# Kernel optimization log

Hardware: AMD Instinct MI355X
Metric: run time of the kernel (lower is better)

Reference implementation:

```python
import jax, jax.numpy as jnp
import numpy as np

HID, FFN, E, K = 1024, 4096, 8, 2
CAP_FACTOR = 1.25


def setup_inputs() -> dict:
    key = jax.random.key(0)
    k1, k2, k3, k4 = jax.random.split(key, 4)
    B, T = 4, 2048
    x = jax.random.normal(k1, (B, T, HID), dtype=jnp.float32)
    router_w = jax.random.normal(k2, (E, HID), dtype=jnp.float32) * 0.02
    w1 = jax.random.normal(k3, (E, HID, FFN), dtype=jnp.float32) * 0.02
    w2 = jax.random.normal(k4, (E, FFN, HID), dtype=jnp.float32) * 0.02
    return {"x": x, "router_w": router_w, "w1": w1, "w2": w2}


def reference(x, router_w, w1, w2):
    B, T, H = x.shape
    N = B * T
    x_flat = x.reshape(N, H)
    # capacity per expert (static, shape-derived)
    C = max(1, int(CAP_FACTOR * N / E * K))

    # router (eval mode: no noise)
    logits = x_flat @ router_w.T                      # [N, E]
    probs = jax.nn.softmax(logits, axis=-1)
    top_v, top_i = jax.lax.top_k(probs, K)            # [N, K]
    top_v = top_v / jnp.sum(top_v, axis=-1, keepdims=True)

    out = jnp.zeros_like(x_flat)
    for k in range(K):
        eid = top_i[:, k]                             # [N] expert id per token
        gate = top_v[:, k]                            # [N]
        # position of each token within its expert, in token order
        onehot = jax.nn.one_hot(eid, E, dtype=jnp.int32)          # [N, E]
        pos = jnp.take_along_axis(jnp.cumsum(onehot, axis=0), eid[:, None], axis=1)[:, 0] - 1
        keep = pos < C                                # capacity drop (first C in token order)
        slot = jnp.where(keep, eid * C + pos, E * C)  # dropped tokens -> dump slot

        # dispatch: scatter kept tokens into per-expert capacity buffers
        buf = jnp.zeros((E * C + 1, H), dtype=x.dtype).at[slot].add(
            x_flat * keep[:, None].astype(x.dtype))
        expert_in = buf[: E * C].reshape(E, C, H)     # [E, C, H]

        # per-expert FFN (grouped GEMM -> GELU -> grouped GEMM)
        h = jax.nn.gelu(jnp.einsum('ech,ehf->ecf', expert_in, w1), approximate=False)
        y = jnp.einsum('ecf,efh->ech', h, w2)         # [E, C, H]

        # combine: gather back to token order, mask dropped, apply gate
        tok = y.reshape(E * C, H)[jnp.minimum(slot, E * C - 1)]
        out = out + tok * (gate * keep.astype(x.dtype))[:, None]

    return out.reshape(B, T, H)
```

## Files before the change

kernel.cpp:

```cpp
#include <hip/hip_runtime.h>
#include <hip/hip_bf16.h>
#include <math.h>

#define N_TOK 8192
#define HIDD  1024
#define FFND  4096
#define NE    8
#define CAP   2560
#define TMX   20
#define RMAX  16512
#define PBLK  128

typedef __attribute__((ext_vector_type(4))) float  f32x4;
typedef __attribute__((ext_vector_type(8))) __bf16 bf16x8;

__device__ __forceinline__ unsigned short f2bf(float f) {
    unsigned u = __float_as_uint(f);
    u = (u + 0x7fffu + ((u >> 16) & 1u)) >> 16;
    return (unsigned short)u;
}

__device__ __forceinline__ void gld_lds16(const void* g, void* l) {
    __builtin_amdgcn_global_load_lds(
        (const __attribute__((address_space(1))) unsigned int*)g,
        (__attribute__((address_space(3))) unsigned int*)l, 16, 0, 0);
}

template <int R, int C>
__global__ __launch_bounds__(256) void transpose_cvt(const float* __restrict__ W,
                                                     unsigned short* __restrict__ Wt) {
    __shared__ unsigned short st[64][72];
    int e  = blockIdx.z;
    int r0 = blockIdx.y * 64, c0 = blockIdx.x * 64;
    int tid = threadIdx.x;
    int rb = tid >> 4, cq = tid & 15;
    const float* src = W + ((size_t)e * R + r0) * C + c0;
#pragma unroll
    for (int i = 0; i < 4; i++) {
        int kr = i * 16 + rb;
        float4 v = *reinterpret_cast<const float4*>(src + (size_t)kr * C + cq * 4);
        st[cq * 4 + 0][kr] = f2bf(v.x);
        st[cq * 4 + 1][kr] = f2bf(v.y);
        st[cq * 4 + 2][kr] = f2bf(v.z);
        st[cq * 4 + 3][kr] = f2bf(v.w);
    }
    __syncthreads();
    unsigned short* dst = Wt + ((size_t)e * C + c0) * R + r0;
#pragma unroll
    for (int i = 0; i < 4; i++) {
        int cr = i * 16 + rb;
        uint2 v = *reinterpret_cast<const uint2*>(&st[cr][cq * 4]);
        *reinterpret_cast<uint2*>(dst + (size_t)cr * R + cq * 4) = v;
    }
}

__global__ __launch_bounds__(256) void router_kernel(const float* __restrict__ x,
                                                     const float* __restrict__ rw,
                                                     unsigned short* __restrict__ xbf,
                                                     int* __restrict__ cnt,
                                                     int* __restrict__ tok,
                                                     float* __restrict__ gate) {
    __shared__ float4 rwl[2048];
    __shared__ int   e0s[32], e1s[32];
    __shared__ float g0s[32], g1s[32];
    __shared__ int   baseS[16];

    int tid = threadIdx.x, lane = tid & 63, w = tid >> 6;
    for (int i = tid; i < 2048; i += 256) rwl[i] = reinterpret_cast<const float4*>(rw)[i];
    __syncthreads();

    int tbase = blockIdx.x * 32 + w * 8;
    for (int i = 0; i < 8; i++) {
        int t = tbase + i;
        const float4* xr = reinterpret_cast<const float4*>(x) + (size_t)t * 256;
        float4 xv[4];
#pragma unroll
        for (int c = 0; c < 4; c++) xv[c] = xr[c * 64 + lane];
        uint2* xb = reinterpret_cast<uint2*>(xbf) + (size_t)t * 256;
#pragma unroll
        for (int c = 0; c < 4; c++) {
            uint2 p;
            p.x = (unsigned)f2bf(xv[c].x) | ((unsigned)f2bf(xv[c].y) << 16);
            p.y = (unsigned)f2bf(xv[c].z) | ((unsigned)f2bf(xv[c].w) << 16);
            xb[c * 64 + lane] = p;
        }
        float dot[NE];
#pragma unroll
        for (int e = 0; e < NE; e++) {
            float s = 0.f;
#pragma unroll
            for (int c = 0; c < 4; c++) {
                float4 a = rwl[e * 256 + c * 64 + lane];
                s += xv[c].x * a.x + xv[c].y * a.y + xv[c].z * a.z + xv[c].w * a.w;
            }
            dot[e] = s;
        }
#pragma unroll
        for (int e = 0; e < NE; e++) {
            float v = dot[e];
#pragma unroll
            for (int o = 32; o > 0; o >>= 1) v += __shfl_xor(v, o, 64);
            dot[e] = v;
        }
        if (lane == 0) {
            int e0 = 0; float l0 = dot[0];
#pragma unroll
            for (int e = 1; e < NE; e++) if (dot[e] > l0) { l0 = dot[e]; e0 = e; }
            int e1 = -1; float l1 = -3.4e38f;
#pragma unroll
            for (int e = 0; e < NE; e++) if (e != e0 && dot[e] > l1) { l1 = dot[e]; e1 = e; }
            float g0 = 1.f / (1.f + expf(l1 - l0));
            int j = w * 8 + i;
            e0s[j] = e0; e1s[j] = e1; g0s[j] = g0; g1s[j] = 1.f - g0;
        }
    }
    __syncthreads();

    int e0 = 255, e1 = 255, rank0 = 0, rank1 = 0, slotcnt = 0;
    float g0 = 0.f, g1 = 0.f;
    if (w == 0) {
        if (lane < 32) { e0 = e0s[lane]; e1 = e1s[lane]; g0 = g0s[lane]; g1 = g1s[lane]; }
        unsigned long long lt = (1ull << lane) - 1ull;
#pragma unroll
        for (int ee = 0; ee < NE; ee++) {
            unsigned long long m0 = __ballot(e0 == ee);
            unsigned long long m1 = __ballot(e1 == ee);
            if (e0 == ee) rank0 = (int)__popcll(m0 & lt);
            if (e1 == ee) rank1 = (int)__popcll(m1 & lt);
            if (lane == ee)      slotcnt = (int)__popcll(m0);
            if (lane == NE + ee) slotcnt = (int)__popcll(m1);
        }
        if (lane < 16) baseS[lane] = atomicAdd(&cnt[lane * 16], slotcnt);
    }
    __syncthreads();
    if (w == 0 && lane < 32) {
        int t = blockIdx.x * 32 + lane;
        int p0 = baseS[e0] + rank0;
        if (p0 < CAP) { tok[e0 * CAP + p0] = t; gate[e0 * CAP + p0] = g0; }
        int p1 = baseS[NE + e1] + rank1;
        if (p1 < CAP) { tok[(NE + e1) * CAP + p1] = t; gate[(NE + e1) * CAP + p1] = g1; }
    }
}

template <int KD, int ND, int KS, int CH, bool G1>
__global__ __launch_bounds__(256, 4) void ffn_gemm_p(const unsigned short* __restrict__ A,
                                                     const unsigned short* __restrict__ Bw,
                                                     unsigned short* __restrict__ H,
                                                     float* __restrict__ O,
                                                     const int* __restrict__ cntAll,
                                                     const int* __restrict__ tokL,
                                                     const float* __restrict__ gateL) {
    constexpr int TN    = ND / 128;
    constexpr int UNITS = TN * KS;
    constexpr int KDS   = KD / KS;

    __shared__ __align__(16) unsigned short At[128 * 32];
    __shared__ __align__(16) unsigned short Bt[128 * 32];

    int e  = blockIdx.x & 7;
    int pb = blockIdx.x >> 3;

    int cnt0 = min(cntAll[e * 16], CAP);
    int cnt1 = min(cntAll[(e + 8) * 16], CAP);
    int tmx0 = (cnt0 + 127) >> 7, tmx1 = (cnt1 + 127) >> 7;
    int tmsum = tmx0 + tmx1;
    if (tmsum == 0) return;
    int per_chunk = tmsum * CH;
    int total = tmsum * UNITS;

    int offA = 0, offB = 0;
#pragma unroll
    for (int t = 0; t < 16; t++) {
        int cc = min(cntAll[t * 16], CAP);
        if (t < e)     offA += cc;
        if (t < e + 8) offB += cc;
    }

    int tid = threadIdx.x;
    int w = tid >> 6, l = tid & 63;
    int wr = w >> 1, wc = w & 1;

    int r1 = tid >> 2, q1 = tid & 3;
    int r2 = r1 + 64;
    int sw1 = ((q1 ^ ((r1 >> 1) & 3)) << 4);
    int sw2 = ((q1 ^ ((r2 >> 1) & 3)) << 4);
    char* aDst1 = (char*)At + w * 1024;
    char* aDst2 = aDst1 + 4096;
    char* bDst1 = (char*)Bt + w * 1024;
    char* bDst2 = bDst1 + 4096;

    int aro[4], bro[4];
#pragma unroll
    for (int m = 0; m < 4; m++) {
        int rr = wr * 64 + m * 16 + (l & 15);
        aro[m] = rr * 64 + (((l >> 4) ^ ((rr >> 1) & 3)) << 4);
        int cc = wc * 64 + m * 16 + (l & 15);
        bro[m] = cc * 64 + (((l >> 4) ^ ((cc >> 1) & 3)) << 4);
    }

    for (int u0 = pb; u0 < total; u0 += PBLK) {
        int c = u0 / per_chunk;
        int r = u0 - c * per_chunk;
        int s, tm, cnt_e, off_e;
        if (r < tmx0 * CH) { s = e;     tm = r / CH; r -= tm * CH; cnt_e = cnt0; off_e = offA; }
        else { r -= tmx0 * CH; s = e + 8; tm = r / CH; r -= tm * CH; cnt_e = cnt1; off_e = offB; }
        int u  = c * CH + r;
        int tn = (KS > 1) ? (u / KS) : u;
        int ks = (KS > 1) ? (u % KS) : 0;
        const int lbase = s * CAP;

        const char* aSrc1;
        const char* aSrc2;
        if (G1) {
            int p1 = tm * 128 + r1, p2 = tm * 128 + r2;
            int t1 = tokL[lbase + (p1 < cnt_e ? p1 : 0)];
            int t2 = tokL[lbase + (p2 < cnt_e ? p2 : 0)];
            aSrc1 = (const char*)(A + (size_t)t1 * KD + ks * KDS) + sw1;
            aSrc2 = (const char*)(A + (size_t)t2 * KD + ks * KDS) + sw2;
        } else {
            size_t row1 = (size_t)off_e + tm * 128 + r1;
            aSrc1 = (const char*)(A + row1 * KD + ks * KDS) + sw1;
            aSrc2 = (const char*)(A + (row1 + 64) * KD + ks * KDS) + sw2;
        }
        const char* bSrc1 = (const char*)(Bw + ((size_t)e * ND + tn * 128 + r1) * KD + ks * KDS) + sw1;
        const char* bSrc2 = (const char*)(Bw + ((size_t)e * ND + tn * 128 + r2) * KD + ks * KDS) + sw2;

        f32x4 acc[4][4];
#pragma unroll
        for (int m = 0; m < 4; m++)
#pragma unroll
            for (int n = 0; n < 4; n++) acc[m][n] = (f32x4){0.f, 0.f, 0.f, 0.f};

        for (int k0 = 0; k0 < KDS; k0 += 32) {
            size_t kb = (size_t)k0 * 2;
            gld_lds16(aSrc1 + kb, aDst1);
            gld_lds16(aSrc2 + kb, aDst2);
            gld_lds16(bSrc1 + kb, bDst1);
            gld_lds16(bSrc2 + kb, bDst2);
            __syncthreads();
            bf16x8 af[4], bf[4];
#pragma unroll
            for (int m = 0; m < 4; m++) af[m] = *reinterpret_cast<const bf16x8*>((const char*)At + aro[m]);
#pragma unroll
            for (int n = 0; n < 4; n++) bf[n] = *reinterpret_cast<const bf16x8*>((const char*)Bt + bro[n]);
#pragma unroll
            for (int m = 0; m < 4; m++)
#pragma unroll
                for (int n = 0; n < 4; n++)
                    acc[m][n] = __builtin_amdgcn_mfma_f32_16x16x32_bf16(af[m], bf[n], acc[m][n], 0, 0, 0);
            __syncthreads();
        }

        if (G1) {
#pragma unroll
            for (int m = 0; m < 4; m++) {
#pragma unroll
                for (int j = 0; j < 4; j++) {
                    int rr = wr * 64 + m * 16 + (l >> 4) * 4 + j;
                    int p = tm * 128 + rr;
                    if (p < cnt_e) {
                        unsigned short* hp = H + (size_t)(off_e + p) * ND + tn * 128 + wc * 64 + (l & 15);
#pragma unroll
                        for (int n = 0; n < 4; n++) {
                            float v = acc[m][n][j];
                            float g = 0.5f * v * (1.f + erff(v * 0.70710678118654752f));
                            hp[n * 16] = f2bf(g);
                        }
                    }
                }
            }
        } else {
#pragma unroll
            for (int m = 0; m < 4; m++) {
#pragma unroll
                for (int j = 0; j < 4; j++) {
                    int rr = wr * 64 + m * 16 + (l >> 4) * 4 + j;
                    int p = tm * 128 + rr;
                    if (p < cnt_e) {
                        int t = tokL[lbase + p];
                        float gv = gateL[lbase + p];
                        float* op = O + (size_t)t * ND + tn * 128 + wc * 64 + (l & 15);
#pragma unroll
                        for (int n = 0; n < 4; n++) atomicAdd(op + n * 16, gv * acc[m][n][j]);
                    }
                }
            }
        }
    }
}

template <int KD, int ND, bool G1>
__global__ __launch_bounds__(256) void ffn_gemm(const unsigned short* __restrict__ A,
                                                const float* __restrict__ W,
                                                unsigned short* __restrict__ H,
                                                float* __restrict__ O,
                                                const int* __restrict__ cntAll,
                                                const int* __restrict__ tokL,
                                                const float* __restrict__ gateL,
                                                int slot0, int pbase) {
    constexpr int TN = ND / 128;
    int bid = blockIdx.x;
    int tn  = bid % TN;
    int tme = bid / TN;
    int tm  = tme % TMX;
    int s   = slot0 + tme / TMX;
    int eW  = s & 7;
    int cnt_e = min(cntAll[s * 16], CAP);
    if (tm * 128 >= cnt_e) return;
    int off_e = 0;
#pragma unroll
    for (int i = 0; i < 16; i++) {
        int c = min(cntAll[i * 16], CAP);
        off_e += (i >= pbase && i < s) ? c : 0;
    }
    const int lbase = s * CAP;

    __shared__ __align__(16) unsigned short At[128 * 32];
    __shared__ __align__(16) unsigned short Bt[128 * 32];

    int tid = threadIdx.x;
    int w = tid >> 6, l = tid & 63;
    int wr = w >> 1, wc = w & 1;

    int r1 = tid >> 2, q1 = tid & 3;
    int r2 = r1 + 64;
    const char* aSrc1;
    const char* aSrc2;
    if (G1) {
        int p1 = tm * 128 + r1, p2 = tm * 128 + r2;
        int t1 = tokL[lbase + (p1 < cnt_e ? p1 : 0)];
        int t2 = tokL[lbase + (p2 < cnt_e ? p2 : 0)];
        aSrc1 = (const char*)(A + (size_t)t1 * KD) + ((q1 ^ ((r1 >> 1) & 3)) << 4);
        aSrc2 = (const char*)(A + (size_t)t2 * KD) + ((q1 ^ ((r2 >> 1) & 3)) << 4);
    } else {
        size_t row1 = (size_t)off_e + tm * 128 + r1;
        size_t row2 = row1 + 64;
        aSrc1 = (const char*)(A + row1 * KD) + ((q1 ^ ((r1 >> 1) & 3)) << 4);
        aSrc2 = (const char*)(A + row2 * KD) + ((q1 ^ ((r2 >> 1) & 3)) << 4);
    }
    char* aDst1 = (char*)At + w * 1024;
    char* aDst2 = aDst1 + 4096;

    const float* bSrc[4];
    int bOff[16];
#pragma unroll
    for (int j = 0; j < 4; j++) {
        int fidx = j * 1024 + tid * 4;
        int kk = fidx >> 7, n = fidx & 127;
        bSrc[j] = W + (size_t)eW * KD * ND + (size_t)kk * ND + tn * 128 + n;
#pragma unroll
        for (int i = 0; i < 4; i++) {
            int nn = n + i;
            bOff[j * 4 + i] = nn * 64 + ((((kk >> 3) ^ ((nn >> 1) & 3))) << 4) + ((kk & 7) << 1);
        }
    }

    int aro[4], bro[4];
#pragma unroll
    for (int m = 0; m < 4; m++) {
        int rr = wr * 64 + m * 16 + (l & 15);
        aro[m] = rr * 64 + (((l >> 4) ^ ((rr >> 1) & 3)) << 4);
        int cc = wc * 64 + m * 16 + (l & 15);
        bro[m] = cc * 64 + (((l >> 4) ^ ((cc >> 1) & 3)) << 4);
    }

    f32x4 zf = {0.f, 0.f, 0.f, 0.f};
    f32x4 acc[4][4];
#pragma unroll
    for (int m = 0; m < 4; m++)
#pragma unroll
        for (int n = 0; n < 4; n++) acc[m][n] = zf;

    for (int k0 = 0; k0 < KD; k0 += 32) {
        gld_lds16(aSrc1 + (size_t)k0 * 2, aDst1);
        gld_lds16(aSrc2 + (size_t)k0 * 2, aDst2);
        float4 bv[4];
#pragma unroll
        for (int j = 0; j < 4; j++) bv[j] = *reinterpret_cast<const float4*>(bSrc[j] + (size_t)k0 * ND);
        char* btc = (char*)Bt;
#pragma unroll
        for (int j = 0; j < 4; j++) {
            *(unsigned short*)(btc + bOff[j * 4 + 0]) = f2bf(bv[j].x);
            *(unsigned short*)(btc + bOff[j * 4 + 1]) = f2bf(bv[j].y);
            *(unsigned short*)(btc + bOff[j * 4 + 2]) = f2bf(bv[j].z);
            *(unsigned short*)(btc + bOff[j * 4 + 3]) = f2bf(bv[j].w);
        }
        __syncthreads();
        bf16x8 af[4], bf[4];
#pragma unroll
        for (int m = 0; m < 4; m++) af[m] = *reinterpret_cast<const bf16x8*>((const char*)At + aro[m]);
#pragma unroll
        for (int n = 0; n < 4; n++) bf[n] = *reinterpret_cast<const bf16x8*>((const char*)Bt + bro[n]);
#pragma unroll
        for (int m = 0; m < 4; m++)
#pragma unroll
            for (int n = 0; n < 4; n++)
                acc[m][n] = __builtin_amdgcn_mfma_f32_16x16x32_bf16(af[m], bf[n], acc[m][n], 0, 0, 0);
        __syncthreads();
    }

    if (G1) {
#pragma unroll
        for (int m = 0; m < 4; m++) {
#pragma unroll
            for (int j = 0; j < 4; j++) {
                int rr = wr * 64 + m * 16 + (l >> 4) * 4 + j;
                int p = tm * 128 + rr;
                if (p < cnt_e) {
                    size_t row = (size_t)(off_e + p);
                    unsigned short* hp = H + row * ND + tn * 128 + wc * 64 + (l & 15);
#pragma unroll
                    for (int n = 0; n < 4; n++) {
                        float v = acc[m][n][j];
                        float g = 0.5f * v * (1.f + erff(v * 0.70710678118654752f));
                        hp[n * 16] = f2bf(g);
                    }
                }
            }
        }
    } else {
#pragma unroll
        for (int m = 0; m < 4; m++) {
#pragma unroll
            for (int j = 0; j < 4; j++) {
                int rr = wr * 64 + m * 16 + (l >> 4) * 4 + j;
                int p = tm * 128 + rr;
                if (p < cnt_e) {
                    int t = tokL[lbase + p];
                    float gv = gateL[lbase + p];
                    float* op = O + (size_t)t * ND + tn * 128 + wc * 64 + (l & 15);
#pragma unroll
                    for (int n = 0; n < 4; n++) atomicAdd(op + n * 16, gv * acc[m][n][j]);
                }
            }
        }
    }
}

extern "C" void kernel_launch(void* const* d_in, const int* in_sizes, int n_in,
                              void* d_out, int out_size, void* d_ws, size_t ws_size,
                              hipStream_t stream) {
    const float* x  = (const float*)d_in[0];
    const float* rw = (const float*)d_in[1];
    const float* w1 = (const float*)d_in[2];
    const float* w2 = (const float*)d_in[3];
    float* out = (float*)d_out;
    char* ws = (char*)d_ws;

    int*   cnt  = (int*)ws;
    int*   tok  = (int*)(ws + 4096);
    float* gate = (float*)(ws + 4096 + 16 * CAP * 4);
    unsigned short* xbf = (unsigned short*)(ws + (1 << 20));
    size_t hOff = (1 << 20) + (size_t)N_TOK * HIDD * 2;
    unsigned short* h = (unsigned short*)(ws + hOff);

    size_t w1tSz = (size_t)NE * HIDD * FFND * 2;
    size_t hBig = (size_t)RMAX * FFND * 2;
    size_t needBig = hOff + hBig + 2 * w1tSz;

    hipMemsetAsync(cnt, 0, 1024, stream);
    hipMemsetAsync(d_out, 0, (size_t)N_TOK * HIDD * 4, stream);

    hipLaunchKernelGGL(router_kernel, dim3(N_TOK / 32), dim3(256), 0, stream,
                       x, rw, xbf, cnt, tok, gate);

    if (ws_size >= needBig) {
        unsigned short* w1t = (unsigned short*)(ws + hOff + hBig);
        unsigned short* w2t = (unsigned short*)(ws + hOff + hBig + w1tSz);
        hipLaunchKernelGGL((transpose_cvt<HIDD, FFND>), dim3(FFND / 64, HIDD / 64, NE), dim3(256), 0, stream, w1, w1t);
        hipLaunchKernelGGL((transpose_cvt<FFND, HIDD>), dim3(HIDD / 64, FFND / 64, NE), dim3(256), 0, stream, w2, w2t);
        hipLaunchKernelGGL((ffn_gemm_p<HIDD, FFND, 1, 8, true>), dim3(8 * PBLK), dim3(256), 0, stream,
                           xbf, w1t, h, (float*)nullptr, cnt, tok, gate);
        hipLaunchKernelGGL((ffn_gemm_p<FFND, HIDD, 2, 4, false>), dim3(8 * PBLK), dim3(256), 0, stream,
                           h, w2t, (unsigned short*)nullptr, out, cnt, tok, gate);
    } else {
        for (int k = 0; k < 2; k++) {
            hipLaunchKernelGGL((ffn_gemm<HIDD, FFND, true>), dim3(8 * TMX * (FFND / 128)), dim3(256), 0, stream,
                               xbf, w1, h, (float*)nullptr, cnt, tok, gate, 8 * k, 8 * k);
            hipLaunchKernelGGL((ffn_gemm<FFND, HIDD, false>), dim3(8 * TMX * (HIDD / 128)), dim3(256), 0, stream,
                               h, w2, (unsigned short*)nullptr, out, cnt, tok, gate, 8 * k, 8 * k);
        }
    }
}
```

Measured before the change: 542.1 us.

## Replace atomic down-proj combine with two ordered store/add passes and polynomial GELU

```diff
diff --git a/kernel.cpp b/kernel.cpp
--- a/kernel.cpp
+++ b/kernel.cpp
@@ -10,6 +10,7 @@
 #define TMX   20
 #define RMAX  16512
 #define PBLK  128
+#define PBLK2 64
 
 typedef __attribute__((ext_vector_type(4))) float  f32x4;
 typedef __attribute__((ext_vector_type(8))) __bf16 bf16x8;
@@ -18,6 +19,17 @@
     unsigned u = __float_as_uint(f);
     u = (u + 0x7fffu + ((u >> 16) & 1u)) >> 16;
     return (unsigned short)u;
+}
+
+__device__ __forceinline__ float gelu_f(float v) {
+    float x  = v * 0.70710678118654752f;
+    float ax = fabsf(x);
+    float t  = 1.0f / (1.0f + 0.3275911f * ax);
+    float poly = ((((1.061405429f * t - 1.453152027f) * t + 1.421413741f) * t
+                   - 0.284496736f) * t + 0.254829592f) * t;
+    float er = 1.0f - poly * __expf(-x * x);
+    er = copysignf(er, x);
+    return 0.5f * v * (1.0f + er);
 }
 
 __device__ __forceinline__ void gld_lds16(const void* g, void* l) {
@@ -142,14 +154,12 @@
     }
 }
 
-template <int KD, int ND, int KS, int CH, bool G1>
+template <int KD, int ND, int KS, int CH>
 __global__ __launch_bounds__(256, 4) void ffn_gemm_p(const unsigned short* __restrict__ A,
                                                      const unsigned short* __restrict__ Bw,
                                                      unsigned short* __restrict__ H,
-                                                     float* __restrict__ O,
                                                      const int* __restrict__ cntAll,
-                                                     const int* __restrict__ tokL,
-                                                     const float* __restrict__ gateL) {
+                                                     const int* __restrict__ tokL) {
     constexpr int TN    = ND / 128;
     constexpr int UNITS = TN * KS;
     constexpr int KDS   = KD / KS;
@@ -211,16 +221,12 @@
 
         const char* aSrc1;
         const char* aSrc2;
-        if (G1) {
+        {
             int p1 = tm * 128 + r1, p2 = tm * 128 + r2;
             int t1 = tokL[lbase + (p1 < cnt_e ? p1 : 0)];
             int t2 = tokL[lbase + (p2 < cnt_e ? p2 : 0)];
             aSrc1 = (const char*)(A + (size_t)t1 * KD + ks * KDS) + sw1;
             aSrc2 = (const char*)(A + (size_t)t2 * KD + ks * KDS) + sw2;
-        } else {
-            size_t row1 = (size_t)off_e + tm * 128 + r1;
-            aSrc1 = (const char*)(A + row1 * KD + ks * KDS) + sw1;
-            aSrc2 = (const char*)(A + (row1 + 64) * KD + ks * KDS) + sw2;
         }
         const char* bSrc1 = (const char*)(Bw + ((size_t)e * ND + tn * 128 + r1) * KD + ks * KDS) + sw1;
         const char* bSrc2 = (const char*)(Bw + ((size_t)e * ND + tn * 128 + r2) * KD + ks * KDS) + sw2;
@@ -251,37 +257,126 @@
             __syncthreads();
         }
 
-        if (G1) {
-#pragma unroll
-            for (int m = 0; m < 4; m++) {
-#pragma unroll
-                for (int j = 0; j < 4; j++) {
-                    int rr = wr * 64 + m * 16 + (l >> 4) * 4 + j;
-                    int p = tm * 128 + rr;
-                    if (p < cnt_e) {
-                        unsigned short* hp = H + (size_t)(off_e + p) * ND + tn * 128 + wc * 64 + (l & 15);
-#pragma unroll
-                        for (int n = 0; n < 4; n++) {
-                            float v = acc[m][n][j];
-                            float g = 0.5f * v * (1.f + erff(v * 0.70710678118654752f));
-                            hp[n * 16] = f2bf(g);
-                        }
-                    }
+#pragma unroll
+        for (int m = 0; m < 4; m++) {
+#pragma unroll
+            for (int j = 0; j < 4; j++) {
+                int rr = wr * 64 + m * 16 + (l >> 4) * 4 + j;
+                int p = tm * 128 + rr;
+                if (p < cnt_e) {
+                    unsigned short* hp = H + (size_t)(off_e + p) * ND + tn * 128 + wc * 64 + (l & 15);
+#pragma unroll
+                    for (int n = 0; n < 4; n++) hp[n * 16] = f2bf(gelu_f(acc[m][n][j]));
                 }
             }
-        } else {
-#pragma unroll
-            for (int m = 0; m < 4; m++) {
-#pragma unroll
-                for (int j = 0; j < 4; j++) {
-                    int rr = wr * 64 + m * 16 + (l >> 4) * 4 + j;
-                    int p = tm * 128 + rr;
-                    if (p < cnt_e) {
-                        int t = tokL[lbase + p];
-                        float gv = gateL[lbase + p];
-                        float* op = O + (size_t)t * ND + tn * 128 + wc * 64 + (l & 15);
-#pragma unroll
-                        for (int n = 0; n < 4; n++) atomicAdd(op + n * 16, gv * acc[m][n][j]);
+        }
+    }
+}
+
+template <int KD, int ND, int CH, bool ADD>
+__global__ __launch_bounds__(256, 4) void ffn_gemm_p2(const unsigned short* __restrict__ A,
+                                                      const unsigned short* __restrict__ Bw,
+                                                      float* __restrict__ O,
+                                                      const int* __restrict__ cntAll,
+                                                      const int* __restrict__ tokL,
+                                                      const float* __restrict__ gateL) {
+    constexpr int TN   = ND / 128;
+    constexpr int SGRP = ADD ? 8 : 0;
+
+    __shared__ __align__(16) unsigned short At[128 * 32];
+    __shared__ __align__(16) unsigned short Bt[128 * 32];
+
+    int e  = blockIdx.x & 7;
+    int pb = blockIdx.x >> 3;
+    int s  = e + SGRP;
+
+    int cnt_e = min(cntAll[s * 16], CAP);
+    int tmx = (cnt_e + 127) >> 7;
+    if (tmx == 0) return;
+    int per_chunk = tmx * CH;
+    int total = tmx * TN;
+
+    int off_e = 0;
+#pragma unroll
+    for (int t = 0; t < 16; t++) off_e += (t < s) ? min(cntAll[t * 16], CAP) : 0;
+    const int lbase = s * CAP;
+
+    int tid = threadIdx.x;
+    int w = tid >> 6, l = tid & 63;
+    int wr = w >> 1, wc = w & 1;
+
+    int r1 = tid >> 2, q1 = tid & 3;
+    int r2 = r1 + 64;
+    int sw1 = ((q1 ^ ((r1 >> 1) & 3)) << 4);
+    int sw2 = ((q1 ^ ((r2 >> 1) & 3)) << 4);
+    char* aDst1 = (char*)At + w * 1024;
+    char* aDst2 = aDst1 + 4096;
+    char* bDst1 = (char*)Bt + w * 1024;
+    char* bDst2 = bDst1 + 4096;
+
+    int aro[4], bro[4];
+#pragma unroll
+    for (int m = 0; m < 4; m++) {
+        int rr = wr * 64 + m * 16 + (l & 15);
+        aro[m] = rr * 64 + (((l >> 4) ^ ((rr >> 1) & 3)) << 4);
+        int cc = wc * 64 + m * 16 + (l & 15);
+        bro[m] = cc * 64 + (((l >> 4) ^ ((cc >> 1) & 3)) << 4);
+    }
+
+    for (int u0 = pb; u0 < total; u0 += PBLK2) {
+        int c = u0 / per_chunk;
+        int r = u0 - c * per_chunk;
+        int tm = r / CH;
+        int ci = r - tm * CH;
+        int tn = c * CH + ci;
+
+        size_t row1 = (size_t)off_e + tm * 128 + r1;
+        const char* aSrc1 = (const char*)(A + row1 * KD) + sw1;
+        const char* aSrc2 = (const char*)(A + (row1 + 64) * KD) + sw2;
+        const char* bSrc1 = (const char*)(Bw + ((size_t)e * ND + tn * 128 + r1) * KD) + sw1;
+        const char* bSrc2 = (const char*)(Bw + ((size_t)e * ND + tn * 128 + r2) * KD) + sw2;
+
+        f32x4 acc[4][4];
+#pragma unroll
+        for (int m = 0; m < 4; m++)
+#pragma unroll
+            for (int n = 0; n < 4; n++) acc[m][n] = (f32x4){0.f, 0.f, 0.f, 0.f};
+
+        for (int k0 = 0; k0 < KD; k0 += 32) {
+            size_t kb = (size_t)k0 * 2;
+            gld_lds16(aSrc1 + kb, aDst1);
+            gld_lds16(aSrc2 + kb, aDst2);
+            gld_lds16(bSrc1 + kb, bDst1);
+            gld_lds16(bSrc2 + kb, bDst2);
+            __syncthreads();
+            bf16x8 af[4], bf[4];
+#pragma unroll
+            for (int m = 0; m < 4; m++) af[m] = *reinterpret_cast<const bf16x8*>((const char*)At + aro[m]);
+#pragma unroll
+            for (int n = 0; n < 4; n++) bf[n] = *reinterpret_cast<const bf16x8*>((const char*)Bt + bro[n]);
+#pragma unroll
+            for (int m = 0; m < 4; m++)
+#pragma unroll
+                for (int n = 0; n < 4; n++)
+                    acc[m][n] = __builtin_amdgcn_mfma_f32_16x16x32_bf16(af[m], bf[n], acc[m][n], 0, 0, 0);
+            __syncthreads();
+        }
+
+#pragma unroll
+        for (int m = 0; m < 4; m++) {
+#pragma unroll
+            for (int j = 0; j < 4; j++) {
+                int rr = wr * 64 + m * 16 + (l >> 4) * 4 + j;
+                int p = tm * 128 + rr;
+                if (p < cnt_e) {
+                    int t = tokL[lbase + p];
+                    float gv = gateL[lbase + p];
+                    float* op = O + (size_t)t * ND + tn * 128 + wc * 64 + (l & 15);
+#pragma unroll
+                    for (int n = 0; n < 4; n++) {
+                        float v = gv * acc[m][n][j];
+                        if (ADD) op[n * 16] += v;
+                        else     op[n * 16] = v;
                     }
                 }
             }
@@ -410,11 +505,7 @@
                     size_t row = (size_t)(off_e + p);
                     unsigned short* hp = H + row * ND + tn * 128 + wc * 64 + (l & 15);
 #pragma unroll
-                    for (int n = 0; n < 4; n++) {
-                        float v = acc[m][n][j];
-                        float g = 0.5f * v * (1.f + erff(v * 0.70710678118654752f));
-                        hp[n * 16] = f2bf(g);
-                    }
+                    for (int n = 0; n < 4; n++) hp[n * 16] = f2bf(gelu_f(acc[m][n][j]));
                 }
             }
         }
@@ -469,10 +560,12 @@
         unsigned short* w2t = (unsigned short*)(ws + hOff + hBig + w1tSz);
         hipLaunchKernelGGL((transpose_cvt<HIDD, FFND>), dim3(FFND / 64, HIDD / 64, NE), dim3(256), 0, stream, w1, w1t);
         hipLaunchKernelGGL((transpose_cvt<FFND, HIDD>), dim3(HIDD / 64, FFND / 64, NE), dim3(256), 0, stream, w2, w2t);
-        hipLaunchKernelGGL((ffn_gemm_p<HIDD, FFND, 1, 8, true>), dim3(8 * PBLK), dim3(256), 0, stream,
-                           xbf, w1t, h, (float*)nullptr, cnt, tok, gate);
-        hipLaunchKernelGGL((ffn_gemm_p<FFND, HIDD, 2, 4, false>), dim3(8 * PBLK), dim3(256), 0, stream,
-                           h, w2t, (unsigned short*)nullptr, out, cnt, tok, gate);
+        hipLaunchKernelGGL((ffn_gemm_p<HIDD, FFND, 1, 8>), dim3(8 * PBLK), dim3(256), 0, stream,
+                           xbf, w1t, h, cnt, tok);
+        hipLaunchKernelGGL((ffn_gemm_p2<FFND, HIDD, 4, false>), dim3(8 * PBLK2), dim3(256), 0, stream,
+                           h, w2t, out, cnt, tok, gate);
+        hipLaunchKernelGGL((ffn_gemm_p2<FFND, HIDD, 4, true>), dim3(8 * PBLK2), dim3(256), 0, stream,
+                           h, w2t, out, cnt, tok, gate);
     } else {
         for (int k = 0; k < 2; k++) {
             hipLaunchKernelGGL((ffn_gemm<HIDD, FFND, true>), dim3(8 * TMX * (FFND / 128)), dim3(256), 0, stream,
```

Measured after the change: 660.8 us. +21.9%, slower.

## Switch expert GEMMs to 32x32x16 MFMA with K=64 tiles and fast GELU

Applied to the files above, without the earlier changes.

```diff
diff --git a/kernel.cpp b/kernel.cpp
--- a/kernel.cpp
+++ b/kernel.cpp
@@ -11,13 +11,25 @@
 #define RMAX  16512
 #define PBLK  128
 
-typedef __attribute__((ext_vector_type(4))) float  f32x4;
-typedef __attribute__((ext_vector_type(8))) __bf16 bf16x8;
+typedef __attribute__((ext_vector_type(4)))  float  f32x4;
+typedef __attribute__((ext_vector_type(16))) float  f32x16;
+typedef __attribute__((ext_vector_type(8)))  __bf16 bf16x8;
 
 __device__ __forceinline__ unsigned short f2bf(float f) {
     unsigned u = __float_as_uint(f);
     u = (u + 0x7fffu + ((u >> 16) & 1u)) >> 16;
     return (unsigned short)u;
+}
+
+__device__ __forceinline__ float gelu_f(float v) {
+    float x  = v * 0.70710678118654752f;
+    float ax = fabsf(x);
+    float t  = 1.0f / (1.0f + 0.3275911f * ax);
+    float poly = ((((1.061405429f * t - 1.453152027f) * t + 1.421413741f) * t
+                   - 0.284496736f) * t + 0.254829592f) * t;
+    float er = 1.0f - poly * __expf(-x * x);
+    er = copysignf(er, x);
+    return 0.5f * v * (1.0f + er);
 }
 
 __device__ __forceinline__ void gld_lds16(const void* g, void* l) {
@@ -142,8 +154,8 @@
     }
 }
 
-template <int KD, int ND, int KS, int CH, bool G1>
-__global__ __launch_bounds__(256, 4) void ffn_gemm_p(const unsigned short* __restrict__ A,
+template <int KD, int ND, int KS, int CH, bool G1F>
+__global__ __launch_bounds__(256, 4) void ffn_gemm_q(const unsigned short* __restrict__ A,
                                                      const unsigned short* __restrict__ Bw,
                                                      unsigned short* __restrict__ H,
                                                      float* __restrict__ O,
@@ -154,8 +166,8 @@
     constexpr int UNITS = TN * KS;
     constexpr int KDS   = KD / KS;
 
-    __shared__ __align__(16) unsigned short At[128 * 32];
-    __shared__ __align__(16) unsigned short Bt[128 * 32];
+    __shared__ __align__(16) unsigned short At[128 * 64];
+    __shared__ __align__(16) unsigned short Bt[128 * 64];
 
     int e  = blockIdx.x & 7;
     int pb = blockIdx.x >> 3;
@@ -180,22 +192,26 @@
     int w = tid >> 6, l = tid & 63;
     int wr = w >> 1, wc = w & 1;
 
-    int r1 = tid >> 2, q1 = tid & 3;
-    int r2 = r1 + 64;
-    int sw1 = ((q1 ^ ((r1 >> 1) & 3)) << 4);
-    int sw2 = ((q1 ^ ((r2 >> 1) & 3)) << 4);
-    char* aDst1 = (char*)At + w * 1024;
-    char* aDst2 = aDst1 + 4096;
-    char* bDst1 = (char*)Bt + w * 1024;
-    char* bDst2 = bDst1 + 4096;
-
-    int aro[4], bro[4];
-#pragma unroll
-    for (int m = 0; m < 4; m++) {
-        int rr = wr * 64 + m * 16 + (l & 15);
-        aro[m] = rr * 64 + (((l >> 4) ^ ((rr >> 1) & 3)) << 4);
-        int cc = wc * 64 + m * 16 + (l & 15);
-        bro[m] = cc * 64 + (((l >> 4) ^ ((cc >> 1) & 3)) << 4);
+    int sr  = tid >> 3;
+    int ssw = (((tid & 7) ^ ((tid >> 4) & 7)) << 4);
+    char* aD[4];
+    char* bD[4];
+#pragma unroll
+    for (int j = 0; j < 4; j++) {
+        aD[j] = (char*)At + j * 4096 + w * 1024;
+        bD[j] = (char*)Bt + j * 4096 + w * 1024;
+    }
+
+    int l31 = l & 31, hi = l >> 5;
+    int s8  = (l31 >> 1) & 7;
+    int kt[4];
+#pragma unroll
+    for (int kh = 0; kh < 4; kh++) kt[kh] = (((kh * 2 + hi) ^ s8) << 4);
+    int aRdB[2], bRdB[2];
+#pragma unroll
+    for (int mi = 0; mi < 2; mi++) {
+        aRdB[mi] = (wr * 64 + mi * 32 + l31) * 128;
+        bRdB[mi] = (wc * 64 + mi * 32 + l31) * 128;
     }
 
     for (int u0 = pb; u0 < total; u0 += PBLK) {
@@ -209,79 +225,64 @@
         int ks = (KS > 1) ? (u % KS) : 0;
         const int lbase = s * CAP;
 
-        const char* aSrc1;
-        const char* aSrc2;
-        if (G1) {
-            int p1 = tm * 128 + r1, p2 = tm * 128 + r2;
-            int t1 = tokL[lbase + (p1 < cnt_e ? p1 : 0)];
-            int t2 = tokL[lbase + (p2 < cnt_e ? p2 : 0)];
-            aSrc1 = (const char*)(A + (size_t)t1 * KD + ks * KDS) + sw1;
-            aSrc2 = (const char*)(A + (size_t)t2 * KD + ks * KDS) + sw2;
-        } else {
-            size_t row1 = (size_t)off_e + tm * 128 + r1;
-            aSrc1 = (const char*)(A + row1 * KD + ks * KDS) + sw1;
-            aSrc2 = (const char*)(A + (row1 + 64) * KD + ks * KDS) + sw2;
-        }
-        const char* bSrc1 = (const char*)(Bw + ((size_t)e * ND + tn * 128 + r1) * KD + ks * KDS) + sw1;
-        const char* bSrc2 = (const char*)(Bw + ((size_t)e * ND + tn * 128 + r2) * KD + ks * KDS) + sw2;
-
-        f32x4 acc[4][4];
-#pragma unroll
-        for (int m = 0; m < 4; m++)
-#pragma unroll
-            for (int n = 0; n < 4; n++) acc[m][n] = (f32x4){0.f, 0.f, 0.f, 0.f};
-
-        for (int k0 = 0; k0 < KDS; k0 += 32) {
+        const char* aS[4];
+        const char* bS[4];
+#pragma unroll
+        for (int j = 0; j < 4; j++) {
+            int p = tm * 128 + j * 32 + sr;
+            int rowg;
+            if (G1F) rowg = tokL[lbase + (p < cnt_e ? p : 0)];
+            else     rowg = off_e + p;
+            aS[j] = (const char*)(A + (size_t)rowg * KD + ks * KDS) + ssw;
+            bS[j] = (const char*)(Bw + ((size_t)e * ND + tn * 128 + j * 32 + sr) * KD + ks * KDS) + ssw;
+        }
+
+        f32x16 a00 = {0.f}, a01 = {0.f}, a10 = {0.f}, a11 = {0.f};
+#pragma unroll
+        for (int i = 0; i < 16; i++) { a00[i] = 0.f; a01[i] = 0.f; a10[i] = 0.f; a11[i] = 0.f; }
+
+        for (int k0 = 0; k0 < KDS; k0 += 64) {
             size_t kb = (size_t)k0 * 2;
-            gld_lds16(aSrc1 + kb, aDst1);
-            gld_lds16(aSrc2 + kb, aDst2);
-            gld_lds16(bSrc1 + kb, bDst1);
-            gld_lds16(bSrc2 + kb, bDst2);
+#pragma unroll
+            for (int j = 0; j < 4; j++) gld_lds16(aS[j] + kb, aD[j]);
+#pragma unroll
+            for (int j = 0; j < 4; j++) gld_lds16(bS[j] + kb, bD[j]);
             __syncthreads();
-            bf16x8 af[4], bf[4];
-#pragma unroll
-            for (int m = 0; m < 4; m++) af[m] = *reinterpret_cast<const bf16x8*>((const char*)At + aro[m]);
-#pragma unroll
-            for (int n = 0; n < 4; n++) bf[n] = *reinterpret_cast<const bf16x8*>((const char*)Bt + bro[n]);
-#pragma unroll
-            for (int m = 0; m < 4; m++)
-#pragma unroll
-                for (int n = 0; n < 4; n++)
-                    acc[m][n] = __builtin_amdgcn_mfma_f32_16x16x32_bf16(af[m], bf[n], acc[m][n], 0, 0, 0);
+            const char* Atc = (const char*)At;
+            const char* Btc = (const char*)Bt;
+#pragma unroll
+            for (int kh = 0; kh < 4; kh++) {
+                bf16x8 fa0 = *reinterpret_cast<const bf16x8*>(Atc + aRdB[0] + kt[kh]);
+                bf16x8 fa1 = *reinterpret_cast<const bf16x8*>(Atc + aRdB[1] + kt[kh]);
+                bf16x8 fb0 = *reinterpret_cast<const bf16x8*>(Btc + bRdB[0] + kt[kh]);
+                bf16x8 fb1 = *reinterpret_cast<const bf16x8*>(Btc + bRdB[1] + kt[kh]);
+                a00 = __builtin_amdgcn_mfma_f32_32x32x16_bf16(fa0, fb0, a00, 0, 0, 0);
+                a01 = __builtin_amdgcn_mfma_f32_32x32x16_bf16(fa0, fb1, a01, 0, 0, 0);
+                a10 = __builtin_amdgcn_mfma_f32_32x32x16_bf16(fa1, fb0, a10, 0, 0, 0);
+                a11 = __builtin_amdgcn_mfma_f32_32x32x16_bf16(fa1, fb1, a11, 0, 0, 0);
+            }
             __syncthreads();
         }
 
-        if (G1) {
-#pragma unroll
-            for (int m = 0; m < 4; m++) {
-#pragma unroll
-                for (int j = 0; j < 4; j++) {
-                    int rr = wr * 64 + m * 16 + (l >> 4) * 4 + j;
-                    int p = tm * 128 + rr;
-                    if (p < cnt_e) {
-                        unsigned short* hp = H + (size_t)(off_e + p) * ND + tn * 128 + wc * 64 + (l & 15);
-#pragma unroll
-                        for (int n = 0; n < 4; n++) {
-                            float v = acc[m][n][j];
-                            float g = 0.5f * v * (1.f + erff(v * 0.70710678118654752f));
-                            hp[n * 16] = f2bf(g);
-                        }
-                    }
-                }
-            }
-        } else {
-#pragma unroll
-            for (int m = 0; m < 4; m++) {
-#pragma unroll
-                for (int j = 0; j < 4; j++) {
-                    int rr = wr * 64 + m * 16 + (l >> 4) * 4 + j;
-                    int p = tm * 128 + rr;
-                    if (p < cnt_e) {
+#pragma unroll
+        for (int mi = 0; mi < 2; mi++) {
+#pragma unroll
+            for (int reg = 0; reg < 16; reg++) {
+                int rr = wr * 64 + mi * 32 + (reg & 3) + 8 * (reg >> 2) + 4 * hi;
+                int p  = tm * 128 + rr;
+                if (p < cnt_e) {
+                    float v0 = (mi == 0) ? a00[reg] : a10[reg];
+                    float v1 = (mi == 0) ? a01[reg] : a11[reg];
+                    if (G1F) {
+                        unsigned short* hp = H + (size_t)(off_e + p) * ND + tn * 128 + wc * 64 + l31;
+                        hp[0]  = f2bf(gelu_f(v0));
+                        hp[32] = f2bf(gelu_f(v1));
+                    } else {
                         int t = tokL[lbase + p];
                         float gv = gateL[lbase + p];
-                        float* op = O + (size_t)t * ND + tn * 128 + wc * 64 + (l & 15);
-#pragma unroll
-                        for (int n = 0; n < 4; n++) atomicAdd(op + n * 16, gv * acc[m][n][j]);
+                        float* op = O + (size_t)t * ND + tn * 128 + wc * 64 + l31;
+                        atomicAdd(op,      gv * v0);
+                        atomicAdd(op + 32, gv * v1);
                     }
                 }
             }
@@ -410,11 +411,7 @@
                     size_t row = (size_t)(off_e + p);
                     unsigned short* hp = H + row * ND + tn * 128 + wc * 64 + (l & 15);
 #pragma unroll
-                    for (int n = 0; n < 4; n++) {
-                        float v = acc[m][n][j];
-                        float g = 0.5f * v * (1.f + erff(v * 0.70710678118654752f));
-                        hp[n * 16] = f2bf(g);
-                    }
+                    for (int n = 0; n < 4; n++) hp[n * 16] = f2bf(gelu_f(acc[m][n][j]));
                 }
             }
         }
@@ -469,9 +466,9 @@
         unsigned short* w2t = (unsigned short*)(ws + hOff + hBig + w1tSz);
         hipLaunchKernelGGL((transpose_cvt<HIDD, FFND>), dim3(FFND / 64, HIDD / 64, NE), dim3(256), 0, stream, w1, w1t);
         hipLaunchKernelGGL((transpose_cvt<FFND, HIDD>), dim3(HIDD / 64, FFND / 64, NE), dim3(256), 0, stream, w2, w2t);
-        hipLaunchKernelGGL((ffn_gemm_p<HIDD, FFND, 1, 8, true>), dim3(8 * PBLK), dim3(256), 0, stream,
+        hipLaunchKernelGGL((ffn_gemm_q<HIDD, FFND, 1, 8, true>), dim3(8 * PBLK), dim3(256), 0, stream,
                            xbf, w1t, h, (float*)nullptr, cnt, tok, gate);
-        hipLaunchKernelGGL((ffn_gemm_p<FFND, HIDD, 2, 4, false>), dim3(8 * PBLK), dim3(256), 0, stream,
+        hipLaunchKernelGGL((ffn_gemm_q<FFND, HIDD, 2, 4, false>), dim3(8 * PBLK), dim3(256), 0, stream,
                            h, w2t, (unsigned short*)nullptr, out, cnt, tok, gate);
     } else {
         for (int k = 0; k < 2; k++) {
```

Measured after the change: 522.0 us. 3.7% less time.
